# Performance work log

Measured on AMD Instinct MI355X. Metric: run time of the kernel, lower is better.

## Reference

```python
import jax, jax.numpy as jnp
import numpy as np

PCR = np.array([-75.2, -75.2, -2.0, 75.2, 75.2, 4.0], np.float32)
VSZ = np.array([0.1, 0.1, 0.15], np.float32)
RADIUS_ROI = 2.4   # sample_radius_with_roi
NUM_KP = 2048      # num_keypoints
BEV_STRIDE = 8
R_RAW = 0.8        # raw-points ball radius
R_C3 = 1.6         # x_conv3 ball radius


def _roi_valid_mask(pxyz, rois):
    # pxyz: [N,3], rois: [R,7] -> bool [N]; sample_points_with_roi math
    d = jnp.linalg.norm(pxyz[:, None, :] - rois[None, :, 0:3], axis=-1)  # [N,R]
    min_d = d.min(axis=-1)
    ridx = jnp.argmin(d, axis=-1)
    roi_max = jnp.linalg.norm(rois[ridx, 3:6] * 0.5, axis=-1)
    return min_d < roi_max + RADIUS_ROI


def _fps(xyz, valid, k):
    # farthest point sampling restricted to valid points (jit-friendly stand-in
    # for sector_fps: fixed k iterations, invalid points pinned to -inf distance)
    d0 = jnp.where(valid, 1e10, -1e10).astype(jnp.float32)
    def step(d, _):
        i = jnp.argmax(d)
        nd = jnp.sum((xyz - xyz[i]) ** 2, axis=-1)
        return jnp.minimum(d, jnp.where(valid, nd, -1e10)), i
    _, idxs = jax.lax.scan(step, d0, None, length=k)
    return idxs


def _bilinear(im, x, y):
    # im: [H,W,C]; faithful to bilinear_interpolate_torch (clamp then weight)
    H, W = im.shape[0], im.shape[1]
    x0 = jnp.clip(jnp.floor(x).astype(jnp.int32), 0, W - 1)
    x1 = jnp.clip(x0 + 1, 0, W - 1)
    y0 = jnp.clip(jnp.floor(y).astype(jnp.int32), 0, H - 1)
    y1 = jnp.clip(y0 + 1, 0, H - 1)
    Ia, Ib, Ic, Id = im[y0, x0], im[y1, x0], im[y0, x1], im[y1, x1]
    xf0, xf1 = x0.astype(x.dtype), x1.astype(x.dtype)
    yf0, yf1 = y0.astype(y.dtype), y1.astype(y.dtype)
    wa = (xf1 - x) * (yf1 - y)
    wb = (xf1 - x) * (y - yf0)
    wc = (x - xf0) * (yf1 - y)
    wd = (x - xf0) * (y - yf0)
    return Ia * wa[:, None] + Ib * wb[:, None] + Ic * wc[:, None] + Id * wd[:, None]


def _aggregate(kp, sxyz, sfeat, radius, W, b):
    # PointNet-style local aggregation: per-point MLP then radius-masked pooling
    d2 = jnp.sum((kp[:, None, :] - sxyz[None, :, :]) ** 2, axis=-1)  # [K,N]
    m = (d2 < radius * radius).astype(sfeat.dtype)
    f = jax.nn.relu(sfeat @ W + b)  # [N,C_out]
    cnt = jnp.maximum(m.sum(axis=-1, keepdims=True), 1.0)
    return (m @ f) / cnt  # [K,C_out]


def reference(points, bboxes, spatial_features, conv3_points, W_raw, b_raw, W_c3, b_c3, W_fuse, bn_gamma, bn_beta, bn_mean, bn_var):
    pxyz = points[..., 0:3]
    # 1) sectorized proposal-centric keypoint sampling (ROI filter + FPS)
    valid = jax.vmap(_roi_valid_mask)(pxyz, bboxes)
    idxs = jax.vmap(lambda x, v: _fps(x, v, NUM_KP))(pxyz, valid)  # [B,K]
    keypoints = jnp.take_along_axis(pxyz, idxs[..., None], axis=1)  # [B,K,3]
    # 2) BEV bilinear interpolation at keypoints
    xi = (keypoints[..., 0] - PCR[0]) / VSZ[0] / BEV_STRIDE
    yi = (keypoints[..., 1] - PCR[1]) / VSZ[1] / BEV_STRIDE
    bev = jnp.transpose(spatial_features, (0, 2, 3, 1))  # [B,H,W,C]
    bev_feats = jax.vmap(_bilinear)(bev, xi, yi)  # [B,K,256]
    # 3) local aggregation from raw points and x_conv3 voxel centers
    raw_agg = jax.vmap(lambda kp, s: _aggregate(kp, s[:, :3], s[:, 3:], R_RAW, W_raw, b_raw))(keypoints, points)
    c3_agg = jax.vmap(lambda kp, s: _aggregate(kp, s[:, :3], s[:, 3:], R_C3, W_c3, b_c3))(keypoints, conv3_points)
    # 4) fusion: Linear(bias=False) + BatchNorm1d (inference) + ReLU
    feats = jnp.concatenate([bev_feats, raw_agg, c3_agg], axis=-1)
    B, K, C = feats.shape
    x = feats.reshape(B * K, C) @ W_fuse
    x = (x - bn_mean) * jax.lax.rsqrt(bn_var + 1e-5) * bn_gamma + bn_beta
    return jax.nn.relu(x), keypoints


def setup_inputs() -> dict:
    key = jax.random.key(0)
    ks = jax.random.split(key, 12)
    B, N, M, R = 2, 16384, 8192, 128
    lo = jnp.array([-75.2, -75.2, -2.0], jnp.float32)
    span = jnp.array([150.4, 150.4, 6.0], jnp.float32)
    pxyz = jax.random.uniform(ks[0], (B, N, 3)) * span + lo
    pfeat = jax.random.normal(ks[1], (B, N, 2))
    points = jnp.concatenate([pxyz, pfeat], axis=-1)
    ctr = jax.random.uniform(ks[2], (B, R, 3)) * span + lo
    dims = jax.random.uniform(ks[3], (B, R, 3)) * jnp.array([3.0, 2.0, 1.0]) + jnp.array([2.0, 1.5, 1.2])
    yaw = jax.random.uniform(ks[4], (B, R, 1)) * (2.0 * np.pi)
    bboxes = jnp.concatenate([ctr, dims, yaw], axis=-1)
    spatial_features = jax.random.normal(ks[5], (B, 256, 188, 188))
    cxyz = jax.random.uniform(ks[6], (B, M, 3)) * span + lo
    cfeat = jax.random.normal(ks[7], (B, M, 64))
    conv3_points = jnp.concatenate([cxyz, cfeat], axis=-1)
    W_raw = jax.random.normal(ks[8], (2, 32)) * 0.1
    W_c3 = jax.random.normal(ks[9], (64, 64)) * 0.05
    W_fuse = jax.random.normal(ks[10], (256 + 32 + 64, 128)) * 0.05
    return dict(points=points, bboxes=bboxes, spatial_features=spatial_features,
                conv3_points=conv3_points, W_raw=W_raw, b_raw=jnp.zeros(32), W_c3=W_c3,
                b_c3=jnp.zeros(64), W_fuse=W_fuse, bn_gamma=jnp.ones(128),
                bn_beta=jnp.zeros(128), bn_mean=jnp.zeros(128), bn_var=jnp.ones(128))
```

## Files before the change

### kernel.cpp

```cpp
#include <hip/hip_runtime.h>
#include <stdint.h>

#define BN_ 2
#define NPT 16384
#define MPT 8192
#define NROI 128
#define KP 2048

typedef unsigned long long u64;
typedef unsigned u32;
typedef float v2f __attribute__((ext_vector_type(2)));

#define FEATS_LEN (4096*352)
#define CNTR_OFF  (FEATS_LEN)
#define CNTC_OFF  (CNTR_OFF + 4096)
#define FRAW_OFF  (CNTC_OFF + 4096)
#define FRAW_LEN  (BN_*NPT*32)
#define GC3_OFF   (FRAW_OFF + FRAW_LEN)
#define GC3_LEN   (BN_*MPT*64)
#define FLAGS_F_OFF (GC3_OFF + GC3_LEN)
#define PX_OFF    (FLAGS_F_OFF + (BN_*NPT)/4)
#define PY_OFF    (PX_OFF + BN_*NPT)
#define PZ_OFF    (PY_OFF + BN_*NPT)
#define SFT_OFF   (PZ_OFF + BN_*NPT)
#define NPOS      (188*188)
#define SFT_LEN   (BN_*NPOS*256)
#define OUT_KP_OFF (4096*128)

#define FPS_BLOCKS  2
#define GC3_BLOCKS  2048
#define ZERO_BLOCKS 177
#define PTILES      553
#define SFT_BLOCKS  (BN_*4*PTILES)
#define BASE_BLOCKS (FPS_BLOCKS + GC3_BLOCKS + ZERO_BLOCKS)
#define TOTAL_BLOCKS (BASE_BLOCKS + SFT_BLOCKS)

template <int CTRL>
__device__ __forceinline__ u32 dppmov(u32 v) {
    return (u32)__builtin_amdgcn_update_dpp((int)v, (int)v, CTRL, 0xF, 0xF, false);
}
__device__ __forceinline__ u32 wave_umax32_dpp(u32 v) {
#define STG(C) { u32 o = dppmov<C>(v); v = (o > v) ? o : v; }
    STG(0x111) STG(0x112) STG(0x114) STG(0x118) STG(0x142) STG(0x143)
#undef STG
    return (u32)__builtin_amdgcn_readlane((int)v, 63);
}

__device__ __forceinline__ v2f pk_add(v2f a, v2f b) {
    v2f r; asm("v_pk_add_f32 %0, %1, %2" : "=v"(r) : "v"(a), "v"(b)); return r;
}
__device__ __forceinline__ v2f pk_mul(v2f a, v2f b) {
    v2f r; asm("v_pk_mul_f32 %0, %1, %2" : "=v"(r) : "v"(a), "v"(b)); return r;
}

__global__ void k_flags(const float* __restrict__ pts, const float* __restrict__ bbox,
                        unsigned char* __restrict__ flags,
                        const float* __restrict__ Wr, const float* __restrict__ br,
                        float* __restrict__ fraw) {
#pragma clang fp contract(off)
    __shared__ float rx[NROI], ry[NROI], rz[NROI], rt[NROI];
    __shared__ float w0[32], w1[32], bs[32];
    int b = blockIdx.x >> 6;
    int t = threadIdx.x;
    if (t < NROI) {
        const float* rr = bbox + (size_t)(b * NROI + t) * 7;
        rx[t] = rr[0]; ry[t] = rr[1]; rz[t] = rr[2];
        float hx = rr[3] * 0.5f, hy = rr[4] * 0.5f, hz = rr[5] * 0.5f;
        rt[t] = sqrtf(((hx * hx) + (hy * hy)) + (hz * hz)) + 2.4f;
    }
    if (t >= 224) { int c = t - 224; w0[c] = Wr[c]; w1[c] = Wr[32 + c]; bs[c] = br[c]; }
    __syncthreads();
    int p = (blockIdx.x & 63) * 256 + t;
    int n = b * NPT + p;
    const float* pr = pts + (size_t)n * 5;
    float x = pr[0], y = pr[1], z = pr[2];
    float mind = 3.4e38f, th = 0.f;
    for (int r = 0; r < NROI; ++r) {
        float dx = x - rx[r], dy = y - ry[r], dz = z - rz[r];
        float ds = sqrtf(((dx * dx) + (dy * dy)) + (dz * dz));
        if (ds < mind) { mind = ds; th = rt[r]; }
    }
    flags[n] = (mind < th) ? 1 : 0;
    float f3 = pr[3], f4 = pr[4];
    float* fo = fraw + (size_t)n * 32;
#pragma unroll 8
    for (int c = 0; c < 32; ++c)
        fo[c] = fmaxf(fmaf(f3, w0[c], fmaf(f4, w1[c], bs[c])), 0.f);
}

template <int NS>
__device__ __forceinline__ void fps_loop(
    int t, int lane, int w, int V,
    const float* __restrict__ pxg, const float* __restrict__ pyg,
    const float* __restrict__ pzg,
    u64 (*rkey)[8],
    float* kbuf,
    float* __restrict__ kout) {
#pragma clang fp contract(off)
    constexpr int NP = NS / 2;
    v2f px[NP], py[NP], pz[NP];
    float d[NS];
    int base = t * NS;
#pragma unroll
    for (int m = 0; m < NP; ++m) {
        int id0 = base + 2 * m;
        v2f qx = ((const v2f*)pxg)[base / 2 + m];
        v2f qy = ((const v2f*)pyg)[base / 2 + m];
        v2f qz = ((const v2f*)pzg)[base / 2 + m];
        bool in0 = id0 < V, in1 = (id0 + 1) < V;
        px[m].x = in0 ? qx.x : 1e18f;  px[m].y = in1 ? qx.y : 1e18f;
        py[m].x = in0 ? qy.x : 1e18f;  py[m].y = in1 ? qy.y : 1e18f;
        pz[m].x = in0 ? qz.x : 1e18f;  pz[m].y = in1 ? qz.y : 1e18f;
        d[2 * m]     = in0 ? 1e10f : 0.0f;
        d[2 * m + 1] = in1 ? 1e10f : 0.0f;
    }

    float bestD = -3.4e38f; int bestJ = 0;
#pragma unroll
    for (int j = 0; j < NS; ++j)
        if (d[j] > bestD) { bestD = d[j]; bestJ = j; }
    u32 gid = (u32)(base + bestJ);
    u32 ord = __float_as_uint(bestD);
    u32 maxOrd = wave_umax32_dpp(ord);
    u64 eq = __ballot(ord == maxOrd);
    int L = __builtin_ctzll(eq);
    u32 winGid = (u32)__builtin_amdgcn_readlane((int)gid, L);
    if (lane == 0) rkey[0][w] = ((u64)maxOrd << 14) | (u64)(0x3FFFu - winGid);
    __syncthreads();

    for (int k = 0; k < KP; ++k) {
        int p = k & 1;
        const u64* kq = rkey[p];
        u64 c0 = kq[0], c1 = kq[1], c2 = kq[2], c3 = kq[3];
        u64 c4 = kq[4], c5 = kq[5], c6 = kq[6], c7 = kq[7];
        u64 m0 = c0 > c1 ? c0 : c1;
        u64 m1 = c2 > c3 ? c2 : c3;
        u64 m2 = c4 > c5 ? c4 : c5;
        u64 m3 = c6 > c7 ? c6 : c7;
        u64 n0 = m0 > m1 ? m0 : m1;
        u64 n1 = m2 > m3 ? m2 : m3;
        u64 win = n0 > n1 ? n0 : n1;
        u32 wid = 0x3FFFu - ((u32)win & 0x3FFFu);
        float wx = pxg[wid], wy = pyg[wid], wz = pzg[wid];
        if (t == 0) { kbuf[k * 3] = wx; kbuf[k * 3 + 1] = wy; kbuf[k * 3 + 2] = wz; }
        v2f wnx; wnx.x = -wx; wnx.y = -wx;
        v2f wny; wny.x = -wy; wny.y = -wy;
        v2f wnz; wnz.x = -wz; wnz.y = -wz;

        bestD = -3.4e38f; bestJ = 0;
#pragma unroll
        for (int m = 0; m < NP; ++m) {
            v2f dx = pk_add(px[m], wnx);
            v2f dy = pk_add(py[m], wny);
            v2f dz = pk_add(pz[m], wnz);
            v2f s  = pk_mul(dx, dx);
            v2f s2 = pk_mul(dy, dy);
            v2f s3 = pk_mul(dz, dz);
            s = pk_add(s, s2);
            s = pk_add(s, s3);
            float dn0 = fminf(d[2 * m], s.x);
            float dn1 = fminf(d[2 * m + 1], s.y);
            d[2 * m] = dn0; d[2 * m + 1] = dn1;
            if (dn0 > bestD) { bestD = dn0; bestJ = 2 * m; }
            if (dn1 > bestD) { bestD = dn1; bestJ = 2 * m + 1; }
        }
        gid = (u32)(base + bestJ);
        ord = __float_as_uint(bestD);
        maxOrd = wave_umax32_dpp(ord);
        eq = __ballot(ord == maxOrd);
        L = __builtin_ctzll(eq);
        winGid = (u32)__builtin_amdgcn_readlane((int)gid, L);
        if (lane == 0) rkey[p ^ 1][w] = ((u64)maxOrd << 14) | (u64)(0x3FFFu - winGid);
        __syncthreads();
    }
    for (int i = t; i < KP * 3; i += 512) kout[i] = kbuf[i];
}

__global__ void __launch_bounds__(512, 2)
k_fps(const float* __restrict__ pts, const unsigned char* __restrict__ flags,
      float* __restrict__ pxw, float* __restrict__ pyw, float* __restrict__ pzw,
      float* __restrict__ kpOut,
      const float* __restrict__ conv3, const float* __restrict__ Wc,
      const float* __restrict__ bc, float* __restrict__ gc3,
      float* __restrict__ zbase,
      const float* __restrict__ sf, float* __restrict__ sfT) {
#pragma clang fp contract(off)
    __shared__ __align__(16) unsigned char smem[24768];
    int bid = blockIdx.x;
    int t = threadIdx.x;

    if (bid >= BASE_BLOCKS) {
        int tb = bid - BASE_BLOCKS;
        int pt = tb % PTILES;
        int rem = tb / PTILES;
        int kt = rem & 3;
        int bb = rem >> 2;
        int pos0 = pt * 64;
        int k0 = kt * 64;
        float* lds = (float*)smem;
        int g = t >> 6, l = t & 63;
        const float* src = sf + ((size_t)(bb * 256 + k0) * NPOS) + pos0;
#pragma unroll
        for (int i = 0; i < 8; ++i) {
            int kl = g + 8 * i;
            float v = (pos0 + l < NPOS) ? src[(size_t)kl * NPOS + l] : 0.f;
            lds[kl * 65 + l] = v;
        }
        __syncthreads();
        float* dst = sfT + (size_t)bb * NPOS * 256;
#pragma unroll
        for (int i = 0; i < 8; ++i) {
            int pl = g + 8 * i;
            int pos = pos0 + pl;
            if (pos < NPOS)
                dst[(size_t)pos * 256 + k0 + l] = lds[l * 65 + pl];
        }
        return;
    }
    if (bid >= FPS_BLOCKS + GC3_BLOCKS) {
        float4* z4 = (float4*)zbase;
        int idx = (bid - FPS_BLOCKS - GC3_BLOCKS) * 512 + t;
        const int STRIDE = ZERO_BLOCKS * 512;
#pragma unroll
        for (int k = 0; k < 4; ++k)
            z4[idx + k * STRIDE] = make_float4(0.f, 0.f, 0.f, 0.f);
        return;
    }
    if (bid >= FPS_BLOCKS) {
        float* w = (float*)smem;
        float (*rf)[64] = (float(*)[64])(smem + 16384);
        for (int i = t; i < 4096; i += 512) w[i] = Wc[i];
        int r = (bid - FPS_BLOCKS) * 8 + (t >> 6);
        int c = t & 63;
        rf[t >> 6][c] = conv3[(size_t)r * 67 + 3 + c];
        __syncthreads();
        float s = bc[c];
#pragma unroll 8
        for (int k = 0; k < 64; ++k) s = fmaf(rf[t >> 6][k], w[k * 64 + c], s);
        gc3[(size_t)r * 64 + c] = fmaxf(s, 0.f);
        return;
    }

    u64 (*rkey)[8] = (u64(*)[8])smem;
    int* wtot      = (int*)(smem + 128);
    float* kbuf    = (float*)(smem + 160);

    int b = bid;
    int lane = t & 63, w = t >> 6;
    int chunk = t * 32;
    const float* pbase = pts + (size_t)b * NPT * 5;
    const unsigned char* fbase = flags + b * NPT;
    float* pxg = pxw + (size_t)b * NPT;
    float* pyg = pyw + (size_t)b * NPT;
    float* pzg = pzw + (size_t)b * NPT;

    int cnt = 0;
    for (int j = 0; j < 32; ++j) cnt += fbase[chunk + j] ? 1 : 0;
    int incl = cnt;
#pragma unroll
    for (int off = 1; off < 64; off <<= 1) {
        int v = __shfl_up(incl, off, 64);
        if (lane >= off) incl += v;
    }
    if (lane == 63) wtot[w] = incl;
    __syncthreads();
    int waveBase = 0, V = 0;
    for (int i = 0; i < 8; ++i) { int wv = wtot[i]; V += wv; if (i < w) waveBase += wv; }
    int pos = waveBase + incl - cnt;

    for (int j = 0; j < 32; ++j) {
        if (fbase[chunk + j]) {
            const float* pr = pbase + (size_t)(chunk + j) * 5;
            pxg[pos] = pr[0]; pyg[pos] = pr[1]; pzg[pos] = pr[2];
            ++pos;
        }
    }
    __syncthreads();

    float* kout = kpOut + (size_t)b * KP * 3;
    if (V == 0) {
        if (t == 0)
            for (int k = 0; k < KP; ++k) {
                kout[k * 3] = pbase[0]; kout[k * 3 + 1] = pbase[1]; kout[k * 3 + 2] = pbase[2];
            }
        return;
    }
    int jm = (V + 511) >> 9;
    if (jm <= 10)      fps_loop<10>(t, lane, w, V, pxg, pyg, pzg, rkey, kbuf, kout);
    else if (jm <= 12) fps_loop<12>(t, lane, w, V, pxg, pyg, pzg, rkey, kbuf, kout);
    else if (jm <= 14) fps_loop<14>(t, lane, w, V, pxg, pyg, pzg, rkey, kbuf, kout);
    else if (jm <= 16) fps_loop<16>(t, lane, w, V, pxg, pyg, pzg, rkey, kbuf, kout);
    else if (jm <= 24) fps_loop<24>(t, lane, w, V, pxg, pyg, pzg, rkey, kbuf, kout);
    else               fps_loop<32>(t, lane, w, V, pxg, pyg, pzg, rkey, kbuf, kout);
}

__global__ void k_rawagg(const float* __restrict__ pts, const float* __restrict__ kp,
                         const float* __restrict__ fraw, float* __restrict__ feats,
                         float* __restrict__ cntR) {
    __shared__ float sp[2560];
    int bid = blockIdx.x;
    int b = bid >> 7, kb = (bid >> 4) & 7, s = bid & 15;
    int t = threadIdx.x;
    int kk = kb * 256 + t, row = b * KP + kk;
    float kx = kp[row * 3], ky = kp[row * 3 + 1], kz = kp[row * 3 + 2];
    float acc[32];
#pragma unroll
    for (int c = 0; c < 32; ++c) acc[c] = 0.f;
    float cnt = 0.f;
    const float R2 = 0.8f * 0.8f;
    for (int tile = 0; tile < 2; ++tile) {
        int nbase = s * 1024 + tile * 512;
        const float* src = pts + (size_t)(b * NPT + nbase) * 5;
        for (int i = t; i < 2560; i += 256) sp[i] = src[i];
        __syncthreads();
        for (int j = 0; j < 512; ++j) {
            float dx = kx - sp[j * 5], dy = ky - sp[j * 5 + 1], dz = kz - sp[j * 5 + 2];
            float d2 = fmaf(dx, dx, fmaf(dy, dy, dz * dz));
            if (d2 < R2) {
                cnt += 1.f;
                const float* fp = fraw + (size_t)(b * NPT + nbase + j) * 32;
#pragma unroll
                for (int c = 0; c < 32; ++c) acc[c] += fp[c];
            }
        }
        __syncthreads();
    }
    float* dst = feats + (size_t)row * 352 + 256;
#pragma unroll
    for (int c = 0; c < 32; ++c) if (acc[c] != 0.f) atomicAdd(dst + c, acc[c]);
    if (cnt != 0.f) atomicAdd(cntR + row, cnt);
}

__global__ void k_c3agg(const float* __restrict__ conv3, const float* __restrict__ kp,
                        const float* __restrict__ gc3, float* __restrict__ feats,
                        float* __restrict__ cntC) {
    __shared__ float sq[256 * 3];
    int bid = blockIdx.x;
    int b = bid >> 7, kb = (bid >> 4) & 7, s = bid & 15;
    int t = threadIdx.x;
    int kk = kb * 256 + t, row = b * KP + kk;
    float kx = kp[row * 3], ky = kp[row * 3 + 1], kz = kp[row * 3 + 2];
    float acc[64];
#pragma unroll
    for (int c = 0; c < 64; ++c) acc[c] = 0.f;
    float cnt = 0.f;
    const float R2 = 1.6f * 1.6f;
    for (int tile = 0; tile < 2; ++tile) {
        int nbase = s * 512 + tile * 256;
        const float* src = conv3 + (size_t)(b * MPT + nbase + t) * 67;
        sq[t * 3] = src[0]; sq[t * 3 + 1] = src[1]; sq[t * 3 + 2] = src[2];
        __syncthreads();
        for (int j = 0; j < 256; ++j) {
            float dx = kx - sq[j * 3], dy = ky - sq[j * 3 + 1], dz = kz - sq[j * 3 + 2];
            float d2 = fmaf(dx, dx, fmaf(dy, dy, dz * dz));
            if (d2 < R2) {
                cnt += 1.f;
                const float* gp = gc3 + (size_t)(b * MPT + nbase + j) * 64;
#pragma unroll
                for (int c = 0; c < 64; ++c) acc[c] += gp[c];
            }
        }
        __syncthreads();
    }
    float* dst = feats + (size_t)row * 352 + 288;
#pragma unroll
    for (int c = 0; c < 64; ++c) if (acc[c] != 0.f) atomicAdd(dst + c, acc[c]);
    if (cnt != 0.f) atomicAdd(cntC + row, cnt);
}

__global__ void k_fuse(const float* __restrict__ feats, const float* __restrict__ cntR,
                       const float* __restrict__ cntC, const float* __restrict__ Wf,
                       const float* __restrict__ gma, const float* __restrict__ bta,
                       const float* __restrict__ mean, const float* __restrict__ var,
                       const float* __restrict__ sf, const float* __restrict__ sfT,
                       int useT, const float* __restrict__ kp,
                       float* __restrict__ out) {
    __shared__ float a[2][352];
    int r0 = blockIdx.x * 2;
    int t = threadIdx.x;
    for (int i = t; i < 704; i += 256) {
        int rr = i >= 352 ? 1 : 0;
        int k = i - rr * 352;
        int row = r0 + rr;
        float v;
        if (k < 256) {
            const float* kpr = kp + (size_t)row * 3;
            float x = kpr[0], y = kpr[1];
            float xi = ((x - (-75.2f)) / 0.1f) / 8.0f;
            float yi = ((y - (-75.2f)) / 0.1f) / 8.0f;
            int x0 = (int)floorf(xi); x0 = min(max(x0, 0), 187);
            int x1 = min(max(x0 + 1, 0), 187);
            int y0 = (int)floorf(yi); y0 = min(max(y0, 0), 187);
            int y1 = min(max(y0 + 1, 0), 187);
            float xf0 = (float)x0, xf1 = (float)x1, yf0 = (float)y0, yf1 = (float)y1;
            float wa = (xf1 - xi) * (yf1 - yi), wb = (xf1 - xi) * (yi - yf0);
            float wc = (xi - xf0) * (yf1 - yi), wd = (xi - xf0) * (yi - yf0);
            int bb = row >> 11;
            float Ia, Ib, Ic, Id;
            if (useT) {
                const float* bt = sfT + (size_t)bb * NPOS * 256 + k;
                Ia = bt[(size_t)(y0 * 188 + x0) * 256];
                Ib = bt[(size_t)(y1 * 188 + x0) * 256];
                Ic = bt[(size_t)(y0 * 188 + x1) * 256];
                Id = bt[(size_t)(y1 * 188 + x1) * 256];
            } else {
                const float* plane = sf + (size_t)(bb * 256 + k) * NPOS;
                Ia = plane[y0 * 188 + x0]; Ib = plane[y1 * 188 + x0];
                Ic = plane[y0 * 188 + x1]; Id = plane[y1 * 188 + x1];
            }
            v = Ia * wa + Ib * wb + Ic * wc + Id * wd;
        } else {
            v = feats[(size_t)row * 352 + k];
            float cn = (k < 288) ? cntR[row] : cntC[row];
            v = v / fmaxf(cn, 1.0f);
        }
        a[rr][k] = v;
    }
    __syncthreads();
    int r = t >> 7, c = t & 127;
    float s = 0.f;
#pragma unroll 4
    for (int k = 0; k < 352; ++k) s = fmaf(a[r][k], Wf[k * 128 + c], s);
    s = (s - mean[c]) * (1.0f / sqrtf(var[c] + 1e-5f)) * gma[c] + bta[c];
    out[(size_t)(r0 + r) * 128 + c] = fmaxf(s, 0.f);
}

extern "C" void kernel_launch(void* const* d_in, const int* in_sizes, int n_in,
                              void* d_out, int out_size, void* d_ws, size_t ws_size,
                              hipStream_t stream) {
    const float* pts   = (const float*)d_in[0];
    const float* bbox  = (const float*)d_in[1];
    const float* sf    = (const float*)d_in[2];
    const float* conv3 = (const float*)d_in[3];
    const float* Wraw  = (const float*)d_in[4];
    const float* braw  = (const float*)d_in[5];
    const float* Wc3   = (const float*)d_in[6];
    const float* bc3   = (const float*)d_in[7];
    const float* Wf    = (const float*)d_in[8];
    const float* gma   = (const float*)d_in[9];
    const float* bta   = (const float*)d_in[10];
    const float* mean  = (const float*)d_in[11];
    const float* var   = (const float*)d_in[12];

    float* wsf   = (float*)d_ws;
    float* feats = wsf;
    float* cntR  = wsf + CNTR_OFF;
    float* cntC  = wsf + CNTC_OFF;
    float* fraw  = wsf + FRAW_OFF;
    float* gc3   = wsf + GC3_OFF;
    unsigned char* flags = (unsigned char*)(wsf + FLAGS_F_OFF);
    float* pxw   = wsf + PX_OFF;
    float* pyw   = wsf + PY_OFF;
    float* pzw   = wsf + PZ_OFF;
    float* sfT   = wsf + SFT_OFF;

    int useT = (ws_size >= (size_t)(SFT_OFF + SFT_LEN) * sizeof(float)) ? 1 : 0;
    int nblocks = useT ? TOTAL_BLOCKS : BASE_BLOCKS;

    float* outp  = (float*)d_out;
    float* kpOut = outp + OUT_KP_OFF;

    k_flags<<<BN_ * 64, 256, 0, stream>>>(pts, bbox, flags, Wraw, braw, fraw);
    k_fps<<<nblocks, 512, 0, stream>>>(pts, flags, pxw, pyw, pzw, kpOut,
                                       conv3, Wc3, bc3, gc3, wsf, sf, sfT);
    k_rawagg<<<BN_ * 128, 256, 0, stream>>>(pts, kpOut, fraw, feats, cntR);
    k_c3agg<<<BN_ * 128, 256, 0, stream>>>(conv3, kpOut, gc3, feats, cntC);
    k_fuse<<<2048, 256, 0, stream>>>(feats, cntR, cntC, Wf, gma, bta, mean, var,
                                     sf, sfT, useT, kpOut, outp);
}
```

Baseline: 1.909 ms.

## Tree-reduce FPS argmax per thread and merge the two aggregation kernels

Inside the FPS loop, the per-thread serial compare-and-select argmax is replaced by a log-depth fmax tree followed by an equality bitmask tree and ctz, which shortens the dependency chain on each of the 2048 sequential iterations. Separately, the raw-point and conv3 aggregation kernels are merged into one launch with twice the blocks, branching on block index, so both run concurrently and one launch is saved. The tree form adds extra compares and registers, and the merged kernel takes the higher register use of the 64-channel branch.

```diff
diff --git a/kernel.cpp b/kernel.cpp
--- a/kernel.cpp
+++ b/kernel.cpp
@@ -115,17 +115,31 @@
         d[2 * m + 1] = in1 ? 1e10f : 0.0f;
     }
 
-    float bestD = -3.4e38f; int bestJ = 0;
-#pragma unroll
-    for (int j = 0; j < NS; ++j)
-        if (d[j] > bestD) { bestD = d[j]; bestJ = j; }
-    u32 gid = (u32)(base + bestJ);
-    u32 ord = __float_as_uint(bestD);
-    u32 maxOrd = wave_umax32_dpp(ord);
-    u64 eq = __ballot(ord == maxOrd);
-    int L = __builtin_ctzll(eq);
-    u32 winGid = (u32)__builtin_amdgcn_readlane((int)gid, L);
-    if (lane == 0) rkey[0][w] = ((u64)maxOrd << 14) | (u64)(0x3FFFu - winGid);
+    {
+        float tmp[NS];
+#pragma unroll
+        for (int j = 0; j < NS; ++j) tmp[j] = d[j];
+#pragma unroll
+        for (int s = 1; s < NS; s <<= 1)
+#pragma unroll
+            for (int j = 0; j + s < NS; j += 2 * s) tmp[j] = fmaxf(tmp[j], tmp[j + s]);
+        float maxD = tmp[0];
+        u32 bits[NS];
+#pragma unroll
+        for (int j = 0; j < NS; ++j) bits[j] = (d[j] == maxD) ? (1u << j) : 0u;
+#pragma unroll
+        for (int s = 1; s < NS; s <<= 1)
+#pragma unroll
+            for (int j = 0; j + s < NS; j += 2 * s) bits[j] |= bits[j + s];
+        int bestJ = __builtin_ctz(bits[0]);
+        u32 gid = (u32)(base + bestJ);
+        u32 ord = __float_as_uint(maxD);
+        u32 maxOrd = wave_umax32_dpp(ord);
+        u64 eq = __ballot(ord == maxOrd);
+        int L = __builtin_ctzll(eq);
+        u32 winGid = (u32)__builtin_amdgcn_readlane((int)gid, L);
+        if (lane == 0) rkey[0][w] = ((u64)maxOrd << 14) | (u64)(0x3FFFu - winGid);
+    }
     __syncthreads();
 
     for (int k = 0; k < KP; ++k) {
@@ -147,7 +161,7 @@
         v2f wny; wny.x = -wy; wny.y = -wy;
         v2f wnz; wnz.x = -wz; wnz.y = -wz;
 
-        bestD = -3.4e38f; bestJ = 0;
+        float tmp[NS];
 #pragma unroll
         for (int m = 0; m < NP; ++m) {
             v2f dx = pk_add(px[m], wnx);
@@ -161,15 +175,27 @@
             float dn0 = fminf(d[2 * m], s.x);
             float dn1 = fminf(d[2 * m + 1], s.y);
             d[2 * m] = dn0; d[2 * m + 1] = dn1;
-            if (dn0 > bestD) { bestD = dn0; bestJ = 2 * m; }
-            if (dn1 > bestD) { bestD = dn1; bestJ = 2 * m + 1; }
-        }
-        gid = (u32)(base + bestJ);
-        ord = __float_as_uint(bestD);
-        maxOrd = wave_umax32_dpp(ord);
-        eq = __ballot(ord == maxOrd);
-        L = __builtin_ctzll(eq);
-        winGid = (u32)__builtin_amdgcn_readlane((int)gid, L);
+            tmp[2 * m] = dn0; tmp[2 * m + 1] = dn1;
+        }
+#pragma unroll
+        for (int s = 1; s < NS; s <<= 1)
+#pragma unroll
+            for (int j = 0; j + s < NS; j += 2 * s) tmp[j] = fmaxf(tmp[j], tmp[j + s]);
+        float maxD = tmp[0];
+        u32 bits[NS];
+#pragma unroll
+        for (int j = 0; j < NS; ++j) bits[j] = (d[j] == maxD) ? (1u << j) : 0u;
+#pragma unroll
+        for (int s = 1; s < NS; s <<= 1)
+#pragma unroll
+            for (int j = 0; j + s < NS; j += 2 * s) bits[j] |= bits[j + s];
+        int bestJ = __builtin_ctz(bits[0]);
+        u32 gid = (u32)(base + bestJ);
+        u32 ord = __float_as_uint(maxD);
+        u32 maxOrd = wave_umax32_dpp(ord);
+        u64 eq = __ballot(ord == maxOrd);
+        int L = __builtin_ctzll(eq);
+        u32 winGid = (u32)__builtin_amdgcn_readlane((int)gid, L);
         if (lane == 0) rkey[p ^ 1][w] = ((u64)maxOrd << 14) | (u64)(0x3FFFu - winGid);
         __syncthreads();
     }
@@ -294,78 +320,77 @@
     else               fps_loop<32>(t, lane, w, V, pxg, pyg, pzg, rkey, kbuf, kout);
 }
 
-__global__ void k_rawagg(const float* __restrict__ pts, const float* __restrict__ kp,
-                         const float* __restrict__ fraw, float* __restrict__ feats,
-                         float* __restrict__ cntR) {
+__global__ void k_agg(const float* __restrict__ pts, const float* __restrict__ kp,
+                      const float* __restrict__ fraw,
+                      const float* __restrict__ conv3, const float* __restrict__ gc3,
+                      float* __restrict__ feats,
+                      float* __restrict__ cntR, float* __restrict__ cntC) {
     __shared__ float sp[2560];
-    int bid = blockIdx.x;
-    int b = bid >> 7, kb = (bid >> 4) & 7, s = bid & 15;
+    int bid0 = blockIdx.x;
     int t = threadIdx.x;
-    int kk = kb * 256 + t, row = b * KP + kk;
-    float kx = kp[row * 3], ky = kp[row * 3 + 1], kz = kp[row * 3 + 2];
-    float acc[32];
-#pragma unroll
-    for (int c = 0; c < 32; ++c) acc[c] = 0.f;
-    float cnt = 0.f;
-    const float R2 = 0.8f * 0.8f;
-    for (int tile = 0; tile < 2; ++tile) {
-        int nbase = s * 1024 + tile * 512;
-        const float* src = pts + (size_t)(b * NPT + nbase) * 5;
-        for (int i = t; i < 2560; i += 256) sp[i] = src[i];
-        __syncthreads();
-        for (int j = 0; j < 512; ++j) {
-            float dx = kx - sp[j * 5], dy = ky - sp[j * 5 + 1], dz = kz - sp[j * 5 + 2];
-            float d2 = fmaf(dx, dx, fmaf(dy, dy, dz * dz));
-            if (d2 < R2) {
-                cnt += 1.f;
-                const float* fp = fraw + (size_t)(b * NPT + nbase + j) * 32;
-#pragma unroll
-                for (int c = 0; c < 32; ++c) acc[c] += fp[c];
+    if (bid0 < BN_ * 128) {
+        int bid = bid0;
+        int b = bid >> 7, kb = (bid >> 4) & 7, s = bid & 15;
+        int kk = kb * 256 + t, row = b * KP + kk;
+        float kx = kp[row * 3], ky = kp[row * 3 + 1], kz = kp[row * 3 + 2];
+        float acc[32];
+#pragma unroll
+        for (int c = 0; c < 32; ++c) acc[c] = 0.f;
+        float cnt = 0.f;
+        const float R2 = 0.8f * 0.8f;
+        for (int tile = 0; tile < 2; ++tile) {
+            int nbase = s * 1024 + tile * 512;
+            const float* src = pts + (size_t)(b * NPT + nbase) * 5;
+            for (int i = t; i < 2560; i += 256) sp[i] = src[i];
+            __syncthreads();
+            for (int j = 0; j < 512; ++j) {
+                float dx = kx - sp[j * 5], dy = ky - sp[j * 5 + 1], dz = kz - sp[j * 5 + 2];
+                float d2 = fmaf(dx, dx, fmaf(dy, dy, dz * dz));
+                if (d2 < R2) {
+                    cnt += 1.f;
+                    const float* fp = fraw + (size_t)(b * NPT + nbase + j) * 32;
+#pragma unroll
+                    for (int c = 0; c < 32; ++c) acc[c] += fp[c];
+                }
             }
-        }
-        __syncthreads();
-    }
-    float* dst = feats + (size_t)row * 352 + 256;
-#pragma unroll
-    for (int c = 0; c < 32; ++c) if (acc[c] != 0.f) atomicAdd(dst + c, acc[c]);
-    if (cnt != 0.f) atomicAdd(cntR + row, cnt);
-}
-
-__global__ void k_c3agg(const float* __restrict__ conv3, const float* __restrict__ kp,
-                        const float* __restrict__ gc3, float* __restrict__ feats,
-                        float* __restrict__ cntC) {
-    __shared__ float sq[256 * 3];
-    int bid = blockIdx.x;
-    int b = bid >> 7, kb = (bid >> 4) & 7, s = bid & 15;
-    int t = threadIdx.x;
-    int kk = kb * 256 + t, row = b * KP + kk;
-    float kx = kp[row * 3], ky = kp[row * 3 + 1], kz = kp[row * 3 + 2];
-    float acc[64];
-#pragma unroll
-    for (int c = 0; c < 64; ++c) acc[c] = 0.f;
-    float cnt = 0.f;
-    const float R2 = 1.6f * 1.6f;
-    for (int tile = 0; tile < 2; ++tile) {
-        int nbase = s * 512 + tile * 256;
-        const float* src = conv3 + (size_t)(b * MPT + nbase + t) * 67;
-        sq[t * 3] = src[0]; sq[t * 3 + 1] = src[1]; sq[t * 3 + 2] = src[2];
-        __syncthreads();
-        for (int j = 0; j < 256; ++j) {
-            float dx = kx - sq[j * 3], dy = ky - sq[j * 3 + 1], dz = kz - sq[j * 3 + 2];
-            float d2 = fmaf(dx, dx, fmaf(dy, dy, dz * dz));
-            if (d2 < R2) {
-                cnt += 1.f;
-                const float* gp = gc3 + (size_t)(b * MPT + nbase + j) * 64;
-#pragma unroll
-                for (int c = 0; c < 64; ++c) acc[c] += gp[c];
+            __syncthreads();
+        }
+        float* dst = feats + (size_t)row * 352 + 256;
+#pragma unroll
+        for (int c = 0; c < 32; ++c) if (acc[c] != 0.f) atomicAdd(dst + c, acc[c]);
+        if (cnt != 0.f) atomicAdd(cntR + row, cnt);
+    } else {
+        int bid = bid0 - BN_ * 128;
+        int b = bid >> 7, kb = (bid >> 4) & 7, s = bid & 15;
+        int kk = kb * 256 + t, row = b * KP + kk;
+        float kx = kp[row * 3], ky = kp[row * 3 + 1], kz = kp[row * 3 + 2];
+        float acc[64];
+#pragma unroll
+        for (int c = 0; c < 64; ++c) acc[c] = 0.f;
+        float cnt = 0.f;
+        const float R2 = 1.6f * 1.6f;
+        for (int tile = 0; tile < 2; ++tile) {
+            int nbase = s * 512 + tile * 256;
+            const float* src = conv3 + (size_t)(b * MPT + nbase + t) * 67;
+            sp[t * 3] = src[0]; sp[t * 3 + 1] = src[1]; sp[t * 3 + 2] = src[2];
+            __syncthreads();
+            for (int j = 0; j < 256; ++j) {
+                float dx = kx - sp[j * 3], dy = ky - sp[j * 3 + 1], dz = kz - sp[j * 3 + 2];
+                float d2 = fmaf(dx, dx, fmaf(dy, dy, dz * dz));
+                if (d2 < R2) {
+                    cnt += 1.f;
+                    const float* gp = gc3 + (size_t)(b * MPT + nbase + j) * 64;
+#pragma unroll
+                    for (int c = 0; c < 64; ++c) acc[c] += gp[c];
+                }
             }
-        }
-        __syncthreads();
-    }
-    float* dst = feats + (size_t)row * 352 + 288;
-#pragma unroll
-    for (int c = 0; c < 64; ++c) if (acc[c] != 0.f) atomicAdd(dst + c, acc[c]);
-    if (cnt != 0.f) atomicAdd(cntC + row, cnt);
+            __syncthreads();
+        }
+        float* dst = feats + (size_t)row * 352 + 288;
+#pragma unroll
+        for (int c = 0; c < 64; ++c) if (acc[c] != 0.f) atomicAdd(dst + c, acc[c]);
+        if (cnt != 0.f) atomicAdd(cntC + row, cnt);
+    }
 }
 
 __global__ void k_fuse(const float* __restrict__ feats, const float* __restrict__ cntR,
@@ -463,8 +488,8 @@
     k_flags<<<BN_ * 64, 256, 0, stream>>>(pts, bbox, flags, Wraw, braw, fraw);
     k_fps<<<nblocks, 512, 0, stream>>>(pts, flags, pxw, pyw, pzw, kpOut,
                                        conv3, Wc3, bc3, gc3, wsf, sf, sfT);
-    k_rawagg<<<BN_ * 128, 256, 0, stream>>>(pts, kpOut, fraw, feats, cntR);
-    k_c3agg<<<BN_ * 128, 256, 0, stream>>>(conv3, kpOut, gc3, feats, cntC);
+    k_agg<<<BN_ * 256, 256, 0, stream>>>(pts, kpOut, fraw, conv3, gc3,
+                                         feats, cntR, cntC);
     k_fuse<<<2048, 256, 0, stream>>>(feats, cntR, cntC, Wf, gma, bta, mean, var,
                                      sf, sfT, useT, kpOut, outp);
 }
```

Result: no change. 1.904 ms (-0.3%).
